# Kernel tuning notes

Measured on AMD Instinct MI355X. Metric: run time of the kernel, lower is better.

## Reference

```python
import jax, jax.numpy as jnp
import numpy as np

MSE_W, SSIM_W = 0.6, 0.4
WIN, SIGMA = 11, 1.5


def _gaussian_window():
    coords = jnp.arange(WIN, dtype=jnp.float32) - (WIN - 1) / 2.0
    g = jnp.exp(-coords ** 2 / (2.0 * SIGMA ** 2))
    g = g / g.sum()
    w = jnp.outer(g, g)  # [11,11]
    return w.reshape(1, 1, WIN, WIN)  # OIHW


def _blur(x, window):
    # x: [B,1,H,W], valid conv with 11x11 gaussian
    return jax.lax.conv_general_dilated(
        x, window, window_strides=(1, 1), padding='VALID',
        dimension_numbers=('NCHW', 'OIHW', 'NCHW'))


def setup_inputs() -> dict:
    key = jax.random.key(0)
    k1, k2 = jax.random.split(key)
    pred = jax.random.uniform(k1, (32, 1, 512, 512), dtype=jnp.float32)
    target = jax.random.uniform(k2, (32, 1, 512, 512), dtype=jnp.float32)
    return {"pred": pred, "target": target}


def reference(pred, target):
    window = _gaussian_window()
    C1 = (0.01 * 1.0) ** 2
    C2 = (0.03 * 1.0) ** 2

    mse_loss = jnp.mean((pred - target) ** 2)

    mu1 = _blur(pred, window)
    mu2 = _blur(target, window)
    mu1_sq = mu1 * mu1
    mu2_sq = mu2 * mu2
    mu1_mu2 = mu1 * mu2
    sigma1_sq = _blur(pred * pred, window) - mu1_sq
    sigma2_sq = _blur(target * target, window) - mu2_sq
    sigma12 = _blur(pred * target, window) - mu1_mu2

    ssim_map = (2.0 * mu1_mu2 + C1) * (2.0 * sigma12 + C2) / (
        (mu1_sq + mu2_sq + C1) * (sigma1_sq + sigma2_sq + C2) + 1e-6)
    ssim_loss = 1.0 - jnp.mean(ssim_map)

    return MSE_W * mse_loss + SSIM_W * ssim_loss
```

## Files before the change

kernel.cpp:

```cpp
#include <hip/hip_runtime.h>
#include <math.h>

#define BATCH 32
#define H 512
#define W 512
#define OUT_HW 502
#define TS_X 32
#define BAND 32
#define NBANDS 16
#define NTX 16
#define NBLOCKS (NTX * BATCH)
#define N1 ((double)BATCH * H * W)
#define N2 ((double)BATCH * OUT_HW * OUT_HW)

#define RSTR 56
#define TSTR 56

struct GaussW { float g[11]; };

typedef _Float16 h8  __attribute__((ext_vector_type(8)));
typedef __fp16   h2t __attribute__((ext_vector_type(2)));
typedef float    f4t __attribute__((ext_vector_type(4)));

__global__ __launch_bounds__(256, 2)
void ssim_mfma_kernel(const float* __restrict__ pred,
                      const float* __restrict__ targ,
                      float* __restrict__ ws_contrib,
                      GaussW gw)
{
    __shared__ __align__(16) _Float16 raw[4][48 * RSTR];
    __shared__ __align__(16) _Float16 rbt[4][32 * TSTR];
    __shared__ float red[8];

    const int tid = threadIdx.x;
    const int bid = blockIdx.x;
    const int tx  = bid >> 5;
    const int b   = ((bid & 7) << 2) | ((bid >> 3) & 3);
    const int ox0 = tx * TS_X;
    const int cols = min(TS_X, OUT_HW - ox0);
    const bool interior_x = (ox0 + 48 <= W);

    const float* __restrict__ pb = pred + ((size_t)b << 18);
    const float* __restrict__ tb = targ + ((size_t)b << 18);

    const int lane = tid & 63, wave = tid >> 6;
    const int quad = lane >> 4, nn = lane & 15, quad8 = quad << 3;

    const int pr = tid / 6, pg = tid - pr * 6;
    const bool pactive = interior_x | (pg < 4);

    {
        _Float16* base = &raw[0][0];
        const int total = 4 * 48 * RSTR;
        for (int i = tid * 8; i < total; i += 256 * 8)
            *(f4t*)(base + i) = f4t{0.f, 0.f, 0.f, 0.f};
    }

    h8 gfrag;
    #pragma unroll
    for (int j = 0; j < 8; ++j) {
        const int kk = quad8 + j - nn;
        float val = 0.f;
        #pragma unroll
        for (int t2 = 0; t2 < 11; ++t2) val = (kk == t2) ? gw.g[t2] : val;
        gfrag[j] = (_Float16)val;
    }
    const f4t zero4 = {0.f, 0.f, 0.f, 0.f};
    const float C1 = 1e-4f, C2 = 9e-4f;

    float mse_local = 0.f, ssim_local = 0.f;

    auto do_vblur = [&](int out0v) {
        const int c0 = (wave & 1) << 4, r0v = (wave >> 1) << 4;
        f4t dv2[4];
        #pragma unroll
        for (int ch = 0; ch < 4; ++ch) {
            const h8 a = *(const h8*)&rbt[ch][(c0 + nn) * TSTR + r0v + quad8];
            dv2[ch] = __builtin_amdgcn_mfma_f32_16x16x32_f16(a, gfrag, zero4, 0, 0, 0);
        }
        const int rowg = out0v + r0v + nn;
        if (rowg < OUT_HW) {
            #pragma unroll
            for (int reg = 0; reg < 4; ++reg) {
                const int cl = c0 + (quad << 2) + reg;
                if (cl < cols) {
                    const float A = dv2[0][reg], Bv = dv2[1][reg];
                    const float U = dv2[2][reg], V  = dv2[3][reg];
                    const float A2 = A * A, B2 = Bv * Bv;
                    const float mu12_2 = 0.5f * (A2 - B2);
                    const float musq   = 0.5f * (A2 + B2);
                    const float sig12_2 = 0.5f * (U - V) - mu12_2;
                    const float sigsum  = 0.5f * (U + V) - musq;
                    const float num = (mu12_2 + C1) * (sig12_2 + C2);
                    const float den = (musq + C1) * (sigsum + C2) + 1e-6f;
                    ssim_local += num * __builtin_amdgcn_rcpf(den);
                }
            }
        }
    };

    f4t pf0, pf1, pf2, pf3;
    {
        if ((tid < 42 * 6) & pactive) {
            const int base = (pr << 9) + ox0 + 8 * pg;
            pf0 = *(const f4t*)(pb + base);
            pf1 = *(const f4t*)(pb + base + 4);
            pf2 = *(const f4t*)(tb + base);
            pf3 = *(const f4t*)(tb + base + 4);
        }
    }

    __syncthreads();

    int hbase = 0, obase = 0;

    #pragma unroll 1
    for (int band = 0; band < NBANDS; ++band) {
        const int out0 = band * BAND;
        const int h0   = (band == 0) ? 0 : (out0 + 10);
        const int nnew = min(out0 + 42, H) - h0;

        if (band > 0) do_vblur(out0 - BAND);

        if ((tid < nnew * 6) & pactive) {
            const h2t hp0 = __builtin_amdgcn_cvt_pkrtz(pf0[0], pf0[1]);
            const h2t hp1 = __builtin_amdgcn_cvt_pkrtz(pf0[2], pf0[3]);
            const h2t hp2 = __builtin_amdgcn_cvt_pkrtz(pf1[0], pf1[1]);
            const h2t hp3 = __builtin_amdgcn_cvt_pkrtz(pf1[2], pf1[3]);
            const h2t ht0 = __builtin_amdgcn_cvt_pkrtz(pf2[0], pf2[1]);
            const h2t ht1 = __builtin_amdgcn_cvt_pkrtz(pf2[2], pf2[3]);
            const h2t ht2 = __builtin_amdgcn_cvt_pkrtz(pf3[0], pf3[1]);
            const h2t ht3 = __builtin_amdgcn_cvt_pkrtz(pf3[2], pf3[3]);
            __align__(16) h2t sv[4], dv[4], ssv[4], ddv[4];
            sv[0] = hp0 + ht0; sv[1] = hp1 + ht1; sv[2] = hp2 + ht2; sv[3] = hp3 + ht3;
            dv[0] = hp0 - ht0; dv[1] = hp1 - ht1; dv[2] = hp2 - ht2; dv[3] = hp3 - ht3;
            ssv[0] = sv[0] * sv[0]; ssv[1] = sv[1] * sv[1];
            ssv[2] = sv[2] * sv[2]; ssv[3] = sv[3] * sv[3];
            ddv[0] = dv[0] * dv[0]; ddv[1] = dv[1] * dv[1];
            ddv[2] = dv[2] * dv[2]; ddv[3] = dv[3] * dv[3];

            if (pg < 4) {
                const h2t macc = (ddv[0] + ddv[1]) + (ddv[2] + ddv[3]);
                mse_local += (float)macc[0] + (float)macc[1];
            }

            int s = hbase + pr;
            s -= (s >= 48) ? 48 : 0;
            const int off = s * RSTR + 8 * pg;
            *(f4t*)&raw[0][off] = *(const f4t*)sv;
            *(f4t*)&raw[1][off] = *(const f4t*)dv;
            *(f4t*)&raw[2][off] = *(const f4t*)ssv;
            *(f4t*)&raw[3][off] = *(const f4t*)ddv;
        }

        if (band + 1 < NBANDS) {
            const int nh0   = out0 + BAND + 10;
            const int nnnew = min(out0 + BAND + 42, H) - nh0;
            if ((tid < nnnew * 6) & pactive) {
                const int base = ((nh0 + pr) << 9) + ox0 + 8 * pg;
                pf0 = *(const f4t*)(pb + base);
                pf1 = *(const f4t*)(pb + base + 4);
                pf2 = *(const f4t*)(tb + base);
                pf3 = *(const f4t*)(tb + base + 4);
            }
        }
        __syncthreads();

        #pragma unroll
        for (int k = 0; k < 6; ++k) {
            const int j0 = (k & 1) << 4, r0 = (k >> 1) << 4;
            int u = obase + r0 + nn;
            u -= (u >= 48) ? 48 : 0;
            const h8 a = *(const h8*)&raw[wave][u * RSTR + j0 + quad8];
            const f4t dacc = __builtin_amdgcn_mfma_f32_16x16x32_f16(a, gfrag, zero4, 0, 0, 0);
            h2t* wp = (h2t*)&rbt[wave][(j0 + nn) * TSTR + r0 + (quad << 2)];
            wp[0] = __builtin_amdgcn_cvt_pkrtz(dacc[0], dacc[1]);
            wp[1] = __builtin_amdgcn_cvt_pkrtz(dacc[2], dacc[3]);
        }
        __syncthreads();

        hbase += nnew;  hbase -= (hbase >= 48) ? 48 : 0;
        obase += BAND;  obase -= (obase >= 48) ? 48 : 0;
    }

    do_vblur((NBANDS - 1) * BAND);

    #pragma unroll
    for (int off = 32; off > 0; off >>= 1) {
        ssim_local += __shfl_down(ssim_local, off, 64);
        mse_local  += __shfl_down(mse_local,  off, 64);
    }
    if ((tid & 63) == 0) { red[wave] = ssim_local; red[4 + wave] = mse_local; }
    __syncthreads();
    if (tid == 0) {
        const float s = red[0] + red[1] + red[2] + red[3];
        const float m = red[4] + red[5] + red[6] + red[7];
        const double contrib = 0.6 * (double)m / N1 - 0.4 * (double)s / N2;
        ws_contrib[bid] = (float)contrib;
    }
}

__global__ __launch_bounds__(64)
void finalize_kernel(const float* __restrict__ ws_contrib,
                     float* __restrict__ out)
{
    const int tid = threadIdx.x;
    double s = 0.0;
    #pragma unroll
    for (int i = 0; i < NBLOCKS / 64; ++i)
        s += (double)ws_contrib[tid + i * 64];
    #pragma unroll
    for (int off = 32; off > 0; off >>= 1)
        s += __shfl_down(s, off, 64);
    if (tid == 0)
        out[0] = (float)(0.4 + s);
}

extern "C" void kernel_launch(void* const* d_in, const int* in_sizes, int n_in,
                              void* d_out, int out_size, void* d_ws, size_t ws_size,
                              hipStream_t stream)
{
    const float* pred = (const float*)d_in[0];
    const float* targ = (const float*)d_in[1];
    float* out = (float*)d_out;
    float* ws_contrib = (float*)d_ws;

    GaussW gw;
    double g[11], sum = 0.0;
    for (int i = 0; i < 11; ++i) { double x = i - 5.0; g[i] = exp(-x * x / 4.5); sum += g[i]; }
    for (int i = 0; i < 11; ++i) gw.g[i] = (float)(g[i] / sum);

    ssim_mfma_kernel<<<dim3(NBLOCKS), 256, 0, stream>>>(pred, targ, ws_contrib, gw);
    finalize_kernel<<<1, 64, 0, stream>>>(ws_contrib, out);
}
```

Baseline: 102.8 us.

## Reuse horizontally blurred rows across bands via ring buffer in rbt

Makes the horizontal-blur output buffer a 48-row ring, so rows already blurred for the previous band's halo are kept instead of recomputed. After the first two bands only 4 of 6 MFMA tiles per wave run per band. Load and row-count bookkeeping is changed to fetch the rows in different chunks. It uses more shared memory and adds ring-index arithmetic, and the row accounting carries correctness risk.

Result: no change. 104.1 us (+1.3%).

```diff
diff --git a/kernel.cpp b/kernel.cpp
--- a/kernel.cpp
+++ b/kernel.cpp
@@ -29,7 +29,7 @@
                       GaussW gw)
 {
     __shared__ __align__(16) _Float16 raw[4][48 * RSTR];
-    __shared__ __align__(16) _Float16 rbt[4][32 * TSTR];
+    __shared__ __align__(16) _Float16 rbt[4][48 * TSTR];
     __shared__ float red[8];
 
     const int tid = threadIdx.x;
@@ -70,12 +70,14 @@
 
     float mse_local = 0.f, ssim_local = 0.f;
 
-    auto do_vblur = [&](int out0v) {
+    auto do_vblur = [&](int out0v, int vb) {
         const int c0 = (wave & 1) << 4, r0v = (wave >> 1) << 4;
+        int vs = vb + r0v + quad8;
+        vs -= (vs >= 48) ? 48 : 0;
         f4t dv2[4];
         #pragma unroll
         for (int ch = 0; ch < 4; ++ch) {
-            const h8 a = *(const h8*)&rbt[ch][(c0 + nn) * TSTR + r0v + quad8];
+            const h8 a = *(const h8*)&rbt[ch][(c0 + nn) * TSTR + vs];
             dv2[ch] = __builtin_amdgcn_mfma_f32_16x16x32_f16(a, gfrag, zero4, 0, 0, 0);
         }
         const int rowg = out0v + r0v + nn;
@@ -99,6 +101,18 @@
         }
     };
 
+    auto hblur_tile = [&](int obase, int j0, int r0) {
+        int u = obase + r0 + nn;
+        u -= (u >= 48) ? 48 : 0;
+        const h8 a = *(const h8*)&raw[wave][u * RSTR + j0 + quad8];
+        const f4t dacc = __builtin_amdgcn_mfma_f32_16x16x32_f16(a, gfrag, zero4, 0, 0, 0);
+        int ws = obase + r0 + (quad << 2);
+        ws -= (ws >= 48) ? 48 : 0;
+        h2t* wp = (h2t*)&rbt[wave][(j0 + nn) * TSTR + ws];
+        wp[0] = __builtin_amdgcn_cvt_pkrtz(dacc[0], dacc[1]);
+        wp[1] = __builtin_amdgcn_cvt_pkrtz(dacc[2], dacc[3]);
+    };
+
     f4t pf0, pf1, pf2, pf3;
     {
         if ((tid < 42 * 6) & pactive) {
@@ -117,10 +131,13 @@
     #pragma unroll 1
     for (int band = 0; band < NBANDS; ++band) {
         const int out0 = band * BAND;
-        const int h0   = (band == 0) ? 0 : (out0 + 10);
-        const int nnew = min(out0 + 42, H) - h0;
-
-        if (band > 0) do_vblur(out0 - BAND);
+        const int h0   = (band == 0) ? 0 : ((band == 1) ? 42 : (out0 + 16));
+        const int nnew = min(out0 + 48, H) - h0 - ((band == 0) ? 6 : 0);
+
+        if (band > 0) {
+            int vb = obase + 16;  vb -= (vb >= 48) ? 48 : 0;
+            do_vblur(out0 - BAND, vb);
+        }
 
         if ((tid < nnew * 6) & pactive) {
             const h2t hp0 = __builtin_amdgcn_cvt_pkrtz(pf0[0], pf0[1]);
@@ -154,8 +171,8 @@
         }
 
         if (band + 1 < NBANDS) {
-            const int nh0   = out0 + BAND + 10;
-            const int nnnew = min(out0 + BAND + 42, H) - nh0;
+            const int nh0   = (band == 0) ? 42 : (out0 + BAND + 16);
+            const int nnnew = min(out0 + BAND + 48, H) - nh0;
             if ((tid < nnnew * 6) & pactive) {
                 const int base = ((nh0 + pr) << 9) + ox0 + 8 * pg;
                 pf0 = *(const f4t*)(pb + base);
@@ -166,24 +183,22 @@
         }
         __syncthreads();
 
+        if (band < 2) {
+            #pragma unroll
+            for (int k = 0; k < 2; ++k) hblur_tile(obase, k << 4, 0);
+        }
         #pragma unroll
-        for (int k = 0; k < 6; ++k) {
-            const int j0 = (k & 1) << 4, r0 = (k >> 1) << 4;
-            int u = obase + r0 + nn;
-            u -= (u >= 48) ? 48 : 0;
-            const h8 a = *(const h8*)&raw[wave][u * RSTR + j0 + quad8];
-            const f4t dacc = __builtin_amdgcn_mfma_f32_16x16x32_f16(a, gfrag, zero4, 0, 0, 0);
-            h2t* wp = (h2t*)&rbt[wave][(j0 + nn) * TSTR + r0 + (quad << 2)];
-            wp[0] = __builtin_amdgcn_cvt_pkrtz(dacc[0], dacc[1]);
-            wp[1] = __builtin_amdgcn_cvt_pkrtz(dacc[2], dacc[3]);
-        }
+        for (int k = 2; k < 6; ++k) hblur_tile(obase, (k & 1) << 4, (k >> 1) << 4);
         __syncthreads();
 
         hbase += nnew;  hbase -= (hbase >= 48) ? 48 : 0;
         obase += BAND;  obase -= (obase >= 48) ? 48 : 0;
     }
 
-    do_vblur((NBANDS - 1) * BAND);
+    {
+        int vb = obase + 16;  vb -= (vb >= 48) ? 48 : 0;
+        do_vblur((NBANDS - 1) * BAND, vb);
+    }
 
     #pragma unroll
     for (int off = 32; off > 0; off >>= 1) {
```

## Software-pipeline horizontal and vertical blur stages with one barrier per band

Applied to the files above, without the earlier changes.

Restructures the band loop into a three-stage pipeline: each iteration stores a new raw band, runs the horizontal MFMA blur on the previous band and the vertical blur plus SSIM on the band before that. The raw ring grows from 48 to 80 rows and the transposed buffer is double-buffered, so only one __syncthreads is needed per iteration instead of two. The aim is to cut barrier stalls and let the stages overlap. The cost is more LDS (about 64 KB per block), which may limit occupancy, and two extra loop iterations.

Result: no change. 102.7 us (-0.1%).

```diff
diff --git a/kernel.cpp b/kernel.cpp
--- a/kernel.cpp
+++ b/kernel.cpp
@@ -15,6 +15,7 @@
 
 #define RSTR 56
 #define TSTR 56
+#define RING 80
 
 struct GaussW { float g[11]; };
 
@@ -28,8 +29,8 @@
                       float* __restrict__ ws_contrib,
                       GaussW gw)
 {
-    __shared__ __align__(16) _Float16 raw[4][48 * RSTR];
-    __shared__ __align__(16) _Float16 rbt[4][32 * TSTR];
+    __shared__ __align__(16) _Float16 raw[4][RING * RSTR];
+    __shared__ __align__(16) _Float16 rbt[2][4][32 * TSTR];
     __shared__ float red[8];
 
     const int tid = threadIdx.x;
@@ -51,7 +52,7 @@
 
     {
         _Float16* base = &raw[0][0];
-        const int total = 4 * 48 * RSTR;
+        const int total = 4 * RING * RSTR;
         for (int i = tid * 8; i < total; i += 256 * 8)
             *(f4t*)(base + i) = f4t{0.f, 0.f, 0.f, 0.f};
     }
@@ -70,12 +71,12 @@
 
     float mse_local = 0.f, ssim_local = 0.f;
 
-    auto do_vblur = [&](int out0v) {
+    auto do_vblur = [&](int out0v, int pp) {
         const int c0 = (wave & 1) << 4, r0v = (wave >> 1) << 4;
         f4t dv2[4];
         #pragma unroll
         for (int ch = 0; ch < 4; ++ch) {
-            const h8 a = *(const h8*)&rbt[ch][(c0 + nn) * TSTR + r0v + quad8];
+            const h8 a = *(const h8*)&rbt[pp][ch][(c0 + nn) * TSTR + r0v + quad8];
             dv2[ch] = __builtin_amdgcn_mfma_f32_16x16x32_f16(a, gfrag, zero4, 0, 0, 0);
         }
         const int rowg = out0v + r0v + nn;
@@ -112,50 +113,49 @@
 
     __syncthreads();
 
-    int hbase = 0, obase = 0;
+    int hb = 0, ob = 0;
 
     #pragma unroll 1
-    for (int band = 0; band < NBANDS; ++band) {
-        const int out0 = band * BAND;
-        const int h0   = (band == 0) ? 0 : (out0 + 10);
-        const int nnew = min(out0 + 42, H) - h0;
-
-        if (band > 0) do_vblur(out0 - BAND);
-
-        if ((tid < nnew * 6) & pactive) {
-            const h2t hp0 = __builtin_amdgcn_cvt_pkrtz(pf0[0], pf0[1]);
-            const h2t hp1 = __builtin_amdgcn_cvt_pkrtz(pf0[2], pf0[3]);
-            const h2t hp2 = __builtin_amdgcn_cvt_pkrtz(pf1[0], pf1[1]);
-            const h2t hp3 = __builtin_amdgcn_cvt_pkrtz(pf1[2], pf1[3]);
-            const h2t ht0 = __builtin_amdgcn_cvt_pkrtz(pf2[0], pf2[1]);
-            const h2t ht1 = __builtin_amdgcn_cvt_pkrtz(pf2[2], pf2[3]);
-            const h2t ht2 = __builtin_amdgcn_cvt_pkrtz(pf3[0], pf3[1]);
-            const h2t ht3 = __builtin_amdgcn_cvt_pkrtz(pf3[2], pf3[3]);
-            __align__(16) h2t sv[4], dv[4], ssv[4], ddv[4];
-            sv[0] = hp0 + ht0; sv[1] = hp1 + ht1; sv[2] = hp2 + ht2; sv[3] = hp3 + ht3;
-            dv[0] = hp0 - ht0; dv[1] = hp1 - ht1; dv[2] = hp2 - ht2; dv[3] = hp3 - ht3;
-            ssv[0] = sv[0] * sv[0]; ssv[1] = sv[1] * sv[1];
-            ssv[2] = sv[2] * sv[2]; ssv[3] = sv[3] * sv[3];
-            ddv[0] = dv[0] * dv[0]; ddv[1] = dv[1] * dv[1];
-            ddv[2] = dv[2] * dv[2]; ddv[3] = dv[3] * dv[3];
-
-            if (pg < 4) {
-                const h2t macc = (ddv[0] + ddv[1]) + (ddv[2] + ddv[3]);
-                mse_local += (float)macc[0] + (float)macc[1];
-            }
-
-            int s = hbase + pr;
-            s -= (s >= 48) ? 48 : 0;
-            const int off = s * RSTR + 8 * pg;
-            *(f4t*)&raw[0][off] = *(const f4t*)sv;
-            *(f4t*)&raw[1][off] = *(const f4t*)dv;
-            *(f4t*)&raw[2][off] = *(const f4t*)ssv;
-            *(f4t*)&raw[3][off] = *(const f4t*)ddv;
-        }
-
-        if (band + 1 < NBANDS) {
-            const int nh0   = out0 + BAND + 10;
-            const int nnnew = min(out0 + BAND + 42, H) - nh0;
+    for (int it = 0; it < NBANDS + 2; ++it) {
+        if (it >= 2) do_vblur((it - 2) * BAND, it & 1);
+
+        if (it < NBANDS) {
+            const int nnew = (it == 0) ? 42 : ((it == NBANDS - 1) ? 22 : 32);
+            if ((tid < nnew * 6) & pactive) {
+                const h2t hp0 = __builtin_amdgcn_cvt_pkrtz(pf0[0], pf0[1]);
+                const h2t hp1 = __builtin_amdgcn_cvt_pkrtz(pf0[2], pf0[3]);
+                const h2t hp2 = __builtin_amdgcn_cvt_pkrtz(pf1[0], pf1[1]);
+                const h2t hp3 = __builtin_amdgcn_cvt_pkrtz(pf1[2], pf1[3]);
+                const h2t ht0 = __builtin_amdgcn_cvt_pkrtz(pf2[0], pf2[1]);
+                const h2t ht1 = __builtin_amdgcn_cvt_pkrtz(pf2[2], pf2[3]);
+                const h2t ht2 = __builtin_amdgcn_cvt_pkrtz(pf3[0], pf3[1]);
+                const h2t ht3 = __builtin_amdgcn_cvt_pkrtz(pf3[2], pf3[3]);
+                __align__(16) h2t sv[4], dv[4], ssv[4], ddv[4];
+                sv[0] = hp0 + ht0; sv[1] = hp1 + ht1; sv[2] = hp2 + ht2; sv[3] = hp3 + ht3;
+                dv[0] = hp0 - ht0; dv[1] = hp1 - ht1; dv[2] = hp2 - ht2; dv[3] = hp3 - ht3;
+                ssv[0] = sv[0] * sv[0]; ssv[1] = sv[1] * sv[1];
+                ssv[2] = sv[2] * sv[2]; ssv[3] = sv[3] * sv[3];
+                ddv[0] = dv[0] * dv[0]; ddv[1] = dv[1] * dv[1];
+                ddv[2] = dv[2] * dv[2]; ddv[3] = dv[3] * dv[3];
+
+                if (pg < 4) {
+                    const h2t macc = (ddv[0] + ddv[1]) + (ddv[2] + ddv[3]);
+                    mse_local += (float)macc[0] + (float)macc[1];
+                }
+
+                int s = hb + pr;
+                s -= (s >= RING) ? RING : 0;
+                const int off = s * RSTR + 8 * pg;
+                *(f4t*)&raw[0][off] = *(const f4t*)sv;
+                *(f4t*)&raw[1][off] = *(const f4t*)dv;
+                *(f4t*)&raw[2][off] = *(const f4t*)ssv;
+                *(f4t*)&raw[3][off] = *(const f4t*)ddv;
+            }
+        }
+
+        if (it + 1 < NBANDS) {
+            const int nh0   = ((it + 1) << 5) + 10;
+            const int nnnew = (it + 1 == NBANDS - 1) ? 22 : 32;
             if ((tid < nnnew * 6) & pactive) {
                 const int base = ((nh0 + pr) << 9) + ox0 + 8 * pg;
                 pf0 = *(const f4t*)(pb + base);
@@ -164,26 +164,30 @@
                 pf3 = *(const f4t*)(tb + base + 4);
             }
         }
+
+        if ((it >= 1) & (it <= NBANDS)) {
+            const int hbuf = (it - 1) & 1;
+            #pragma unroll
+            for (int k = 0; k < 6; ++k) {
+                const int j0 = (k & 1) << 4, r0 = (k >> 1) << 4;
+                int u = ob + r0 + nn;
+                u -= (u >= RING) ? RING : 0;
+                const h8 a = *(const h8*)&raw[wave][u * RSTR + j0 + quad8];
+                const f4t dacc = __builtin_amdgcn_mfma_f32_16x16x32_f16(a, gfrag, zero4, 0, 0, 0);
+                h2t* wp = (h2t*)&rbt[hbuf][wave][(j0 + nn) * TSTR + r0 + (quad << 2)];
+                wp[0] = __builtin_amdgcn_cvt_pkrtz(dacc[0], dacc[1]);
+                wp[1] = __builtin_amdgcn_cvt_pkrtz(dacc[2], dacc[3]);
+            }
+        }
+
         __syncthreads();
 
-        #pragma unroll
-        for (int k = 0; k < 6; ++k) {
-            const int j0 = (k & 1) << 4, r0 = (k >> 1) << 4;
-            int u = obase + r0 + nn;
-            u -= (u >= 48) ? 48 : 0;
-            const h8 a = *(const h8*)&raw[wave][u * RSTR + j0 + quad8];
-            const f4t dacc = __builtin_amdgcn_mfma_f32_16x16x32_f16(a, gfrag, zero4, 0, 0, 0);
-            h2t* wp = (h2t*)&rbt[wave][(j0 + nn) * TSTR + r0 + (quad << 2)];
-            wp[0] = __builtin_amdgcn_cvt_pkrtz(dacc[0], dacc[1]);
-            wp[1] = __builtin_amdgcn_cvt_pkrtz(dacc[2], dacc[3]);
-        }
-        __syncthreads();
-
-        hbase += nnew;  hbase -= (hbase >= 48) ? 48 : 0;
-        obase += BAND;  obase -= (obase >= 48) ? 48 : 0;
-    }
-
-    do_vblur((NBANDS - 1) * BAND);
+        if (it < NBANDS) {
+            const int nnew = (it == 0) ? 42 : ((it == NBANDS - 1) ? 22 : 32);
+            hb += nnew;  hb -= (hb >= RING) ? RING : 0;
+        }
+        if (it >= 1) { ob += BAND;  ob -= (ob >= RING) ? RING : 0; }
+    }
 
     #pragma unroll
     for (int off = 32; off > 0; off >>= 1) {
```
